# Optimization experiments

Measured on AMD Instinct MI355X. Metric: run time of the kernel, lower is better.

Reference implementation:

```python
import jax, jax.numpy as jnp
import numpy as np

H = 1024
NH = 16
HD = H // NH

def setup_inputs() -> dict:
    key = jax.random.key(0)
    ks = jax.random.split(key, 10)
    s = 1.0 / np.sqrt(H)
    return {
        "hiddenStates": jax.random.normal(ks[0], (2, 2048, H), dtype=jnp.float32),
        "attentionMask": jnp.zeros((2, 1, 1, 2048), dtype=jnp.float32),
        "Wq": jax.random.uniform(ks[1], (H, H), jnp.float32, -s, s),
        "bq": jax.random.uniform(ks[2], (H,), jnp.float32, -s, s),
        "Wk": jax.random.uniform(ks[3], (H, H), jnp.float32, -s, s),
        "bk": jax.random.uniform(ks[4], (H,), jnp.float32, -s, s),
        "Wv": jax.random.uniform(ks[5], (H, H), jnp.float32, -s, s),
        "bv": jax.random.uniform(ks[6], (H,), jnp.float32, -s, s),
        "Wo": jax.random.uniform(ks[7], (H, H), jnp.float32, -s, s),
        "bo": jax.random.uniform(ks[8], (H,), jnp.float32, -s, s),
    }

def _split_heads(x):
    # [B,S,H] -> [B,NH,S,HD]
    b, s, _ = x.shape
    return x.reshape(b, s, NH, HD).transpose(0, 2, 1, 3)

def reference(hiddenStates, attentionMask, Wq, bq, Wk, bk, Wv, bv, Wo, bo):
    q = _split_heads(hiddenStates @ Wq.T + bq)
    k = _split_heads(hiddenStates @ Wk.T + bk)
    v = _split_heads(hiddenStates @ Wv.T + bv)
    scores = jnp.einsum('bhqd,bhkd->bhqk', q, k) / np.sqrt(HD)
    scores = scores + attentionMask
    probs = jax.nn.softmax(scores, axis=-1)  # dropout p=0 -> identity
    ctx = jnp.einsum('bhqk,bhkd->bhqd', probs, v)
    b, _, s, _ = ctx.shape
    ctx = ctx.transpose(0, 2, 1, 3).reshape(b, s, H)
    return ctx @ Wo.T + bo
```

## Files before the change

### kernel.cpp

```cpp
#include <hip/hip_runtime.h>


#define BB   2
#define SS   2048
#define HH   1024
#define NHH  16
#define HDD  64

#define LOG2E 1.4426950408889634f
#define C1    (0.125f * LOG2E)

typedef _Float16 h8 __attribute__((ext_vector_type(8)));
typedef float f32x4 __attribute__((ext_vector_type(4)));
typedef float f32x16 __attribute__((ext_vector_type(16)));
typedef unsigned short us8 __attribute__((ext_vector_type(8)));

static __device__ __forceinline__ unsigned short f2h(float f) {
  return __builtin_bit_cast(unsigned short, (_Float16)f);
}
static __device__ __forceinline__ f32x4 mfma16(us8 a, us8 b, f32x4 c) {
  return __builtin_amdgcn_mfma_f32_16x16x32_f16(
      __builtin_bit_cast(h8, a), __builtin_bit_cast(h8, b), c, 0, 0, 0);
}
static __device__ __forceinline__ f32x16 mfma32(us8 a, us8 b, f32x16 c) {
  return __builtin_amdgcn_mfma_f32_32x32x16_f16(
      __builtin_bit_cast(h8, a), __builtin_bit_cast(h8, b), c, 0, 0, 0);
}
static __device__ __forceinline__ void gload16(const void* g, void* l) {
  __builtin_amdgcn_global_load_lds(
      (const __attribute__((address_space(1))) unsigned int*)g,
      (__attribute__((address_space(3))) unsigned int*)l, 16, 0, 0);
}
static __device__ __forceinline__ float exp2fast(float x) {
  float r; asm("v_exp_f32 %0, %1" : "=v"(r) : "v"(x)); return r;
}
static __device__ __forceinline__ unsigned cvtpkh(float lo, float hi) {
  unsigned r;
  asm("v_cvt_pkrtz_f16_f32 %0, %1, %2" : "=v"(r) : "v"(lo), "v"(hi));
  return r;
}
static __device__ __forceinline__ int fragoff(int lg, int r) {
  return (((lg << 10) + (r << 3)) ^ (lg << 3));
}

__global__ __launch_bounds__(256)
void pack_kernel(const float* __restrict__ X, const float* __restrict__ Wq,
                 const float* __restrict__ Wk, const float* __restrict__ Wv,
                 const float* __restrict__ Wo,
                 unsigned short* __restrict__ Xh,
                 unsigned short* __restrict__ Bh,
                 unsigned short* __restrict__ Oh) {
  const int t = blockIdx.x;
  const float* src; unsigned short* dst;
  int smt, dmt, kt;
  if (t < 1024) { src = X; dst = Xh; smt = t >> 5; dmt = smt; kt = t & 31; }
  else {
    const int u = t - 1024, which = u >> 8, v = u & 255;
    smt = v >> 5; kt = v & 31;
    if (which == 0)      { src = Wq; dst = Bh; dmt = smt; }
    else if (which == 1) { src = Wk; dst = Bh; dmt = smt + 8; }
    else if (which == 2) { src = Wv; dst = Bh; dmt = smt + 16; }
    else                 { src = Wo; dst = Oh; dmt = smt; }
  }
  const size_t tb = ((size_t)(dmt * 32 + kt)) << 12;
#pragma unroll
  for (int it = 0; it < 2; ++it) {
    const int item = it * 256 + threadIdx.x;
    const int r = item >> 2, lg = item & 3;
    const float* sp = &src[(size_t)(smt * 128 + r) * HH + kt * 32 + lg * 8];
    const float4 a = *(const float4*)sp;
    const float4 b = *(const float4*)(sp + 4);
    const float vals[8] = {a.x, a.y, a.z, a.w, b.x, b.y, b.z, b.w};
    us8 h;
#pragma unroll
    for (int e = 0; e < 8; ++e) h[e] = f2h(vals[e]);
    *(us8*)&dst[tb + fragoff(lg, r)] = h;
  }
}

__global__ __launch_bounds__(256, 3)
void qkv_gemm_kernel(const unsigned short* __restrict__ Ah_,
                     const unsigned short* __restrict__ Bh_,
                     const float* __restrict__ bq, const float* __restrict__ bk,
                     const float* __restrict__ bv,
                     unsigned short* __restrict__ qb,
                     unsigned short* __restrict__ kb,
                     unsigned short* __restrict__ vt) {
  __shared__ __align__(16) unsigned short tiles[2][4096];
  const int tid = threadIdx.x, lane = tid & 63, wid = tid >> 6;
  const int l16 = lane & 15, lg = lane >> 4;
  const int wr = wid >> 1, wc = wid & 1;
  const int mt0 = blockIdx.y, nt0 = blockIdx.x;

  const unsigned short* gA = Ah_ + (((size_t)mt0 * 32) << 12);
  const unsigned short* gB = Bh_ + (((size_t)nt0 * 32) << 12);

  f32x4 acc[4][4] = {};
  for (int kt = 0; kt < 32; ++kt) {
    __syncthreads();
    const size_t ko = ((size_t)kt) << 12;
#pragma unroll
    for (int it = 0; it < 2; ++it) {
      const int c = it * 256 + tid;
      gload16(gA + ko + c * 8, (char*)&tiles[0][0] + c * 16);
      gload16(gB + ko + c * 8, (char*)&tiles[1][0] + c * 16);
    }
    __syncthreads();

    us8 a[4], b[4];
#pragma unroll
    for (int t = 0; t < 4; ++t) {
      a[t] = *(const us8*)&tiles[0][fragoff(lg, wr * 64 + t * 16 + l16)];
      b[t] = *(const us8*)&tiles[1][fragoff(lg, wc * 64 + t * 16 + l16)];
    }
#pragma unroll
    for (int mt = 0; mt < 4; ++mt)
#pragma unroll
      for (int nt = 0; nt < 4; ++nt)
        acc[mt][nt] = mfma16(a[mt], b[nt], acc[mt][nt]);
  }

  const int m0 = mt0 * 128, n0 = nt0 * 128;
#pragma unroll
  for (int nt = 0; nt < 4; ++nt) {
    const int col = n0 + wc * 64 + nt * 16 + l16;
    const int which = col >> 10, nn = col & 1023;
    const float bias = (which == 0) ? bq[nn] : ((which == 1) ? bk[nn] : bv[nn]);
    const int h = nn >> 6, d = nn & 63;
#pragma unroll
    for (int mt = 0; mt < 4; ++mt)
#pragma unroll
      for (int reg = 0; reg < 4; ++reg) {
        const int row = m0 + wr * 64 + mt * 16 + lg * 4 + reg;
        const int bi = row >> 11, si = row & 2047;
        const unsigned short v16 = f2h(acc[mt][nt][reg] + bias);
        const size_t head = (size_t)(bi * NHH + h);
        if (which == 0)      qb[(head * SS + si) * HDD + d] = v16;
        else if (which == 1) kb[(head * SS + si) * HDD + d] = v16;
        else                 vt[(head * HDD + d) * SS + si] = v16;
      }
  }
}

__global__ __launch_bounds__(512)
void attn_kernel(const unsigned short* __restrict__ qb,
                 const unsigned short* __restrict__ kbuf,
                 const unsigned short* __restrict__ vt,
                 const float* __restrict__ mask,
                 unsigned short* __restrict__ Ch) {
  __shared__ __align__(16) unsigned short Klds[2][4096];
  __shared__ __align__(16) unsigned short Vlds[2][4096];

  const int tid = threadIdx.x, lane = tid & 63, w = tid >> 6;
  const int q = lane & 31, hi = lane >> 5;
  const int bh = blockIdx.x;
  const int bi = bh >> 4, h = bh & 15;
  const int q0 = blockIdx.y * 256 + w * 32;
  const size_t bhS = (size_t)bh * SS;
  const int qrow = q0 + q;

  us8 qf[4];
#pragma unroll
  for (int ks = 0; ks < 4; ++ks)
    qf[ks] = *(const us8*)&qb[(bhS + qrow) * HDD + ks * 16 + hi * 8];

  f32x16 o0 = {}, o1 = {};
  float mrun = -1e30f, lrun = 0.0f;

#define STAGE(buf, kt_)                                                        \
  {                                                                            \
    const int key0_ = (kt_) * 64;                                              \
    const int row_ = tid >> 3;                                                 \
    const int c16_ = (tid & 7) ^ (row_ & 7);          \
    gload16(&kbuf[(bhS + key0_ + row_) * HDD + c16_ * 8],                      \
            (char*)&Klds[buf][0] + tid * 16);                                  \
    gload16(&vt[((size_t)bh * HDD + row_) * SS + key0_ + c16_ * 8],            \
            (char*)&Vlds[buf][0] + tid * 16);                                  \
  }

  STAGE(0, 0)
  __syncthreads();

  for (int kt = 0; kt < SS / 64; ++kt) {
    const int buf = kt & 1;
    if (kt + 1 < SS / 64) STAGE(buf ^ 1, kt + 1)
    const int key0 = kt * 64;

    f32x16 s0 = {}, s1 = {};
    __builtin_amdgcn_s_setprio(1);
#pragma unroll
    for (int ks = 0; ks < 4; ++ks) {
      const int bc = ks * 32 + hi * 16;
      const char* kb0 = (const char*)&Klds[buf][0];
      const us8 kf0 = *(const us8*)(kb0 + q * 128 + (bc ^ ((q & 7) << 4)));
      const int r1 = 32 + q;
      const us8 kf1 = *(const us8*)(kb0 + r1 * 128 + (bc ^ ((r1 & 7) << 4)));
      s0 = mfma32(kf0, qf[ks], s0);
      s1 = mfma32(kf1, qf[ks], s1);
    }
    __builtin_amdgcn_s_setprio(0);

    float tmax = -1e30f;
#pragma unroll
    for (int g = 0; g < 4; ++g) {
      const float4 m0 = *(const float4*)&mask[bi * SS + key0 + g * 8 + hi * 4];
      const float4 m1 = *(const float4*)&mask[bi * SS + key0 + 32 + g * 8 + hi * 4];
      const float mm0[4] = {m0.x, m0.y, m0.z, m0.w};
      const float mm1[4] = {m1.x, m1.y, m1.z, m1.w};
#pragma unroll
      for (int j = 0; j < 4; ++j) {
        const int reg = g * 4 + j;
        s0[reg] = s0[reg] * C1 + mm0[j] * LOG2E;
        s1[reg] = s1[reg] * C1 + mm1[j] * LOG2E;
        tmax = fmaxf(tmax, fmaxf(s0[reg], s1[reg]));
      }
    }
    tmax = fmaxf(tmax, __shfl_xor(tmax, 32));

    const float mnew = fmaxf(mrun, tmax);
    if (!__all(tmax <= mrun)) {
      const float rsc = exp2fast(mrun - mnew);
      lrun *= rsc;
#pragma unroll
      for (int reg = 0; reg < 16; ++reg) { o0[reg] *= rsc; o1[reg] *= rsc; }
      mrun = mnew;
    }
    const float mb = mnew - 8.0f;
    float ps = 0.0f;
#pragma unroll
    for (int reg = 0; reg < 16; ++reg) {
      s0[reg] = exp2fast(s0[reg] - mb); ps += s0[reg];
      s1[reg] = exp2fast(s1[reg] - mb); ps += s1[reg];
    }
    ps += __shfl_xor(ps, 32);
    lrun += ps;

    us8 pb[4];
    {
      unsigned C[8], Sx[8];
#pragma unroll
      for (int j = 0; j < 8; ++j) C[j] = cvtpkh(s0[2 * j], s0[2 * j + 1]);
#pragma unroll
      for (int j = 0; j < 8; ++j) Sx[j] = (unsigned)__shfl_xor((int)C[j], 32);
      union { unsigned wd[4]; us8 v; } u0, u1;
      u0.wd[0] = hi ? Sx[2] : C[0]; u0.wd[1] = hi ? Sx[3] : C[1];
      u0.wd[2] = hi ? C[2] : Sx[0]; u0.wd[3] = hi ? C[3] : Sx[1];
      u1.wd[0] = hi ? Sx[6] : C[4]; u1.wd[1] = hi ? Sx[7] : C[5];
      u1.wd[2] = hi ? C[6] : Sx[4]; u1.wd[3] = hi ? C[7] : Sx[5];
      pb[0] = u0.v; pb[1] = u1.v;
#pragma unroll
      for (int j = 0; j < 8; ++j) C[j] = cvtpkh(s1[2 * j], s1[2 * j + 1]);
#pragma unroll
      for (int j = 0; j < 8; ++j) Sx[j] = (unsigned)__shfl_xor((int)C[j], 32);
      u0.wd[0] = hi ? Sx[2] : C[0]; u0.wd[1] = hi ? Sx[3] : C[1];
      u0.wd[2] = hi ? C[2] : Sx[0]; u0.wd[3] = hi ? C[3] : Sx[1];
      u1.wd[0] = hi ? Sx[6] : C[4]; u1.wd[1] = hi ? Sx[7] : C[5];
      u1.wd[2] = hi ? C[6] : Sx[4]; u1.wd[3] = hi ? C[7] : Sx[5];
      pb[2] = u0.v; pb[3] = u1.v;
    }

    __builtin_amdgcn_s_setprio(1);
#pragma unroll
    for (int kslice = 0; kslice < 4; ++kslice) {
      const int bc = kslice * 32 + hi * 16;
      const char* vb = (const char*)&Vlds[buf][0];
      const us8 vf0 = *(const us8*)(vb + q * 128 + (bc ^ ((q & 7) << 4)));
      const int r1 = 32 + q;
      const us8 vf1 = *(const us8*)(vb + r1 * 128 + (bc ^ ((r1 & 7) << 4)));
      o0 = mfma32(vf0, pb[kslice], o0);
      o1 = mfma32(vf1, pb[kslice], o1);
    }
    __builtin_amdgcn_s_setprio(0);

    __syncthreads();
  }

  const float rinv = 1.0f / lrun;
  const int m = bi * SS + qrow;
  const int mt = m >> 7, r = m & 127;
#pragma unroll
  for (int db = 0; db < 2; ++db) {
#pragma unroll
    for (int g = 0; g < 4; ++g) {
      const int d0 = db * 32 + g * 8 + hi * 4;
      const int col = h * 64 + d0;
      const int kt2 = col >> 5, lg2 = (col >> 3) & 3, e0 = col & 7;
      const size_t off = (((size_t)(mt * 32 + kt2)) << 12) + fragoff(lg2, r) + e0;
      ushort4 hv;
#pragma unroll
      for (int j = 0; j < 4; ++j)
        ((unsigned short*)&hv)[j] =
            f2h((db ? o1[g * 4 + j] : o0[g * 4 + j]) * rinv);
      *(ushort4*)&Ch[off] = hv;
    }
  }
#undef STAGE
}

__global__ __launch_bounds__(256, 3)
void out_gemm_kernel(const unsigned short* __restrict__ Ah_,
                     const unsigned short* __restrict__ Bh_,
                     const float* __restrict__ bo, float* __restrict__ out) {
  __shared__ __align__(16) unsigned short tiles[2][4096];
  const int tid = threadIdx.x, lane = tid & 63, wid = tid >> 6;
  const int l16 = lane & 15, lg = lane >> 4;
  const int wr = wid >> 1, wc = wid & 1;
  const int mt0 = blockIdx.y, nt0 = blockIdx.x;

  const unsigned short* gA = Ah_ + (((size_t)mt0 * 32) << 12);
  const unsigned short* gB = Bh_ + (((size_t)nt0 * 32) << 12);

  f32x4 acc[4][4] = {};
  for (int kt = 0; kt < 32; ++kt) {
    __syncthreads();
    const size_t ko = ((size_t)kt) << 12;
#pragma unroll
    for (int it = 0; it < 2; ++it) {
      const int c = it * 256 + tid;
      gload16(gA + ko + c * 8, (char*)&tiles[0][0] + c * 16);
      gload16(gB + ko + c * 8, (char*)&tiles[1][0] + c * 16);
    }
    __syncthreads();

    us8 a[4], b[4];
#pragma unroll
    for (int t = 0; t < 4; ++t) {
      a[t] = *(const us8*)&tiles[0][fragoff(lg, wr * 64 + t * 16 + l16)];
      b[t] = *(const us8*)&tiles[1][fragoff(lg, wc * 64 + t * 16 + l16)];
    }
#pragma unroll
    for (int mt = 0; mt < 4; ++mt)
#pragma unroll
      for (int nt = 0; nt < 4; ++nt)
        acc[mt][nt] = mfma16(a[mt], b[nt], acc[mt][nt]);
  }

  const int m0 = mt0 * 128, n0 = nt0 * 128;
#pragma unroll
  for (int nt = 0; nt < 4; ++nt) {
    const int col = n0 + wc * 64 + nt * 16 + l16;
    const float bias = bo[col];
#pragma unroll
    for (int mt = 0; mt < 4; ++mt)
#pragma unroll
      for (int reg = 0; reg < 4; ++reg) {
        const int row = m0 + wr * 64 + mt * 16 + lg * 4 + reg;
        out[(size_t)row * HH + col] = acc[mt][nt][reg] + bias;
      }
  }
}

extern "C" void kernel_launch(void* const* d_in, const int* in_sizes, int n_in,
                              void* d_out, int out_size, void* d_ws, size_t ws_size,
                              hipStream_t stream) {
  const float* X    = (const float*)d_in[0];
  const float* mask = (const float*)d_in[1];
  const float* Wq   = (const float*)d_in[2];
  const float* bq   = (const float*)d_in[3];
  const float* Wk   = (const float*)d_in[4];
  const float* bk   = (const float*)d_in[5];
  const float* Wv   = (const float*)d_in[6];
  const float* bv   = (const float*)d_in[7];
  const float* Wo   = (const float*)d_in[8];
  const float* bo   = (const float*)d_in[9];
  float* out = (float*)d_out;

  unsigned char* w = (unsigned char*)d_ws;
  const size_t MB = 1024 * 1024;
  unsigned short* Xh = (unsigned short*)(w);
  unsigned short* Bh = (unsigned short*)(w + 8 * MB);
  unsigned short* Oh = (unsigned short*)(w + 14 * MB);
  unsigned short* qb = (unsigned short*)(w + 16 * MB);
  unsigned short* kb = (unsigned short*)(w + 24 * MB);
  unsigned short* vt = (unsigned short*)(w + 32 * MB);
  unsigned short* Ch = Xh;

  pack_kernel<<<2048, 256, 0, stream>>>(X, Wq, Wk, Wv, Wo, Xh, Bh, Oh);
  qkv_gemm_kernel<<<dim3(24, 32), 256, 0, stream>>>(Xh, Bh, bq, bk, bv,
                                                    qb, kb, vt);
  attn_kernel<<<dim3(32, 8), 512, 0, stream>>>(qb, kb, vt, mask, Ch);
  out_gemm_kernel<<<dim3(8, 32), 256, 0, stream>>>(Ch, Oh, bo, out);
}
```

Before: 233.4 us.

## Split attention over key halves with combine kernel, stage mask in LDS

Splits the attention key range into two halves, doubling the attention grid from 256 to 512 blocks. Each half writes partial normalized outputs plus running max and sum, and a new combine kernel merges them into the packed layout used by the output GEMM. Several smaller changes ride along: the mask is pre-scaled by log2e in the pack kernel and staged through LDS, the row max uses a tree reduction, P packing uses permlane32_swap instead of shuffles, and V stores are vectorized in the QKV epilogue. The extra kernel launch and the partial-result round trip through memory are the costs traded for better occupancy on a GPU with many compute units.

```diff
diff --git a/kernel.cpp b/kernel.cpp
--- a/kernel.cpp
+++ b/kernel.cpp
@@ -14,9 +14,13 @@
 typedef float f32x4 __attribute__((ext_vector_type(4)));
 typedef float f32x16 __attribute__((ext_vector_type(16)));
 typedef unsigned short us8 __attribute__((ext_vector_type(8)));
+typedef unsigned u32x2 __attribute__((ext_vector_type(2)));
 
 static __device__ __forceinline__ unsigned short f2h(float f) {
   return __builtin_bit_cast(unsigned short, (_Float16)f);
+}
+static __device__ __forceinline__ float h2f(unsigned short h) {
+  return (float)__builtin_bit_cast(_Float16, h);
 }
 static __device__ __forceinline__ f32x4 mfma16(us8 a, us8 b, f32x4 c) {
   return __builtin_amdgcn_mfma_f32_16x16x32_f16(
@@ -39,6 +43,10 @@
   asm("v_cvt_pkrtz_f16_f32 %0, %1, %2" : "=v"(r) : "v"(lo), "v"(hi));
   return r;
 }
+static __device__ __forceinline__ void pl32swap(unsigned& a, unsigned& b) {
+  u32x2 r = __builtin_amdgcn_permlane32_swap(a, b, false, false);
+  a = r[0]; b = r[1];
+}
 static __device__ __forceinline__ int fragoff(int lg, int r) {
   return (((lg << 10) + (r << 3)) ^ (lg << 3));
 }
@@ -46,11 +54,22 @@
 __global__ __launch_bounds__(256)
 void pack_kernel(const float* __restrict__ X, const float* __restrict__ Wq,
                  const float* __restrict__ Wk, const float* __restrict__ Wv,
-                 const float* __restrict__ Wo,
+                 const float* __restrict__ Wo, const float* __restrict__ mask,
                  unsigned short* __restrict__ Xh,
                  unsigned short* __restrict__ Bh,
-                 unsigned short* __restrict__ Oh) {
+                 unsigned short* __restrict__ Oh,
+                 float* __restrict__ maskl) {
   const int t = blockIdx.x;
+  if (t == 2048) {
+    const int i0 = threadIdx.x * 16;
+#pragma unroll
+    for (int j = 0; j < 4; ++j) {
+      float4 v = *(const float4*)&mask[i0 + j * 4];
+      v.x *= LOG2E; v.y *= LOG2E; v.z *= LOG2E; v.w *= LOG2E;
+      *(float4*)&maskl[i0 + j * 4] = v;
+    }
+    return;
+  }
   const float* src; unsigned short* dst;
   int smt, dmt, kt;
   if (t < 1024) { src = X; dst = Xh; smt = t >> 5; dmt = smt; kt = t & 31; }
@@ -128,17 +147,25 @@
     const float bias = (which == 0) ? bq[nn] : ((which == 1) ? bk[nn] : bv[nn]);
     const int h = nn >> 6, d = nn & 63;
 #pragma unroll
-    for (int mt = 0; mt < 4; ++mt)
-#pragma unroll
-      for (int reg = 0; reg < 4; ++reg) {
-        const int row = m0 + wr * 64 + mt * 16 + lg * 4 + reg;
-        const int bi = row >> 11, si = row & 2047;
-        const unsigned short v16 = f2h(acc[mt][nt][reg] + bias);
-        const size_t head = (size_t)(bi * NHH + h);
-        if (which == 0)      qb[(head * SS + si) * HDD + d] = v16;
-        else if (which == 1) kb[(head * SS + si) * HDD + d] = v16;
-        else                 vt[(head * HDD + d) * SS + si] = v16;
+    for (int mt = 0; mt < 4; ++mt) {
+      const int row0 = m0 + wr * 64 + mt * 16 + lg * 4;
+      const int bi = row0 >> 11, si0 = row0 & 2047;
+      const size_t head = (size_t)(bi * NHH + h);
+      if (which == 2) {
+        ushort4 vv;
+#pragma unroll
+        for (int reg = 0; reg < 4; ++reg)
+          ((unsigned short*)&vv)[reg] = f2h(acc[mt][nt][reg] + bias);
+        *(ushort4*)&vt[(head * HDD + d) * SS + si0] = vv;
+      } else {
+#pragma unroll
+        for (int reg = 0; reg < 4; ++reg) {
+          const unsigned short v16 = f2h(acc[mt][nt][reg] + bias);
+          if (which == 0) qb[(head * SS + si0 + reg) * HDD + d] = v16;
+          else            kb[(head * SS + si0 + reg) * HDD + d] = v16;
+        }
       }
+    }
   }
 }
 
@@ -146,16 +173,20 @@
 void attn_kernel(const unsigned short* __restrict__ qb,
                  const unsigned short* __restrict__ kbuf,
                  const unsigned short* __restrict__ vt,
-                 const float* __restrict__ mask,
-                 unsigned short* __restrict__ Ch) {
+                 const float* __restrict__ maskl,
+                 unsigned short* __restrict__ Op,
+                 float2* __restrict__ Ml) {
   __shared__ __align__(16) unsigned short Klds[2][4096];
   __shared__ __align__(16) unsigned short Vlds[2][4096];
+  __shared__ __align__(16) float Mlds[2][64];
 
   const int tid = threadIdx.x, lane = tid & 63, w = tid >> 6;
   const int q = lane & 31, hi = lane >> 5;
   const int bh = blockIdx.x;
   const int bi = bh >> 4, h = bh & 15;
-  const int q0 = blockIdx.y * 256 + w * 32;
+  const int half = blockIdx.y >> 3;
+  const int q0 = (blockIdx.y & 7) * 256 + w * 32;
+  const int kbase = half * (SS / 2);
   const size_t bhS = (size_t)bh * SS;
   const int qrow = q0 + q;
 
@@ -169,22 +200,24 @@
 
 #define STAGE(buf, kt_)                                                        \
   {                                                                            \
-    const int key0_ = (kt_) * 64;                                              \
+    const int key0_ = kbase + (kt_) * 64;                                      \
     const int row_ = tid >> 3;                                                 \
     const int c16_ = (tid & 7) ^ (row_ & 7);          \
     gload16(&kbuf[(bhS + key0_ + row_) * HDD + c16_ * 8],                      \
             (char*)&Klds[buf][0] + tid * 16);                                  \
     gload16(&vt[((size_t)bh * HDD + row_) * SS + key0_ + c16_ * 8],            \
             (char*)&Vlds[buf][0] + tid * 16);                                  \
+    if (tid < 16)                                                              \
+      gload16(&maskl[bi * SS + key0_ + tid * 4],                               \
+              (char*)&Mlds[buf][0] + tid * 16);                                \
   }
 
   STAGE(0, 0)
   __syncthreads();
 
-  for (int kt = 0; kt < SS / 64; ++kt) {
+  for (int kt = 0; kt < 16; ++kt) {
     const int buf = kt & 1;
-    if (kt + 1 < SS / 64) STAGE(buf ^ 1, kt + 1)
-    const int key0 = kt * 64;
+    if (kt + 1 < 16) STAGE(buf ^ 1, kt + 1)
 
     f32x16 s0 = {}, s1 = {};
     __builtin_amdgcn_s_setprio(1);
@@ -200,21 +233,25 @@
     }
     __builtin_amdgcn_s_setprio(0);
 
-    float tmax = -1e30f;
+    float mx0[8], mx1[4];
 #pragma unroll
     for (int g = 0; g < 4; ++g) {
-      const float4 m0 = *(const float4*)&mask[bi * SS + key0 + g * 8 + hi * 4];
-      const float4 m1 = *(const float4*)&mask[bi * SS + key0 + 32 + g * 8 + hi * 4];
-      const float mm0[4] = {m0.x, m0.y, m0.z, m0.w};
-      const float mm1[4] = {m1.x, m1.y, m1.z, m1.w};
+      const float4 m0v = *(const float4*)&Mlds[buf][g * 8 + hi * 4];
+      const float4 m1v = *(const float4*)&Mlds[buf][32 + g * 8 + hi * 4];
+      const float mm0[4] = {m0v.x, m0v.y, m0v.z, m0v.w};
+      const float mm1[4] = {m1v.x, m1v.y, m1v.z, m1v.w};
 #pragma unroll
       for (int j = 0; j < 4; ++j) {
         const int reg = g * 4 + j;
-        s0[reg] = s0[reg] * C1 + mm0[j] * LOG2E;
-        s1[reg] = s1[reg] * C1 + mm1[j] * LOG2E;
-        tmax = fmaxf(tmax, fmaxf(s0[reg], s1[reg]));
+        s0[reg] = s0[reg] * C1 + mm0[j];
+        s1[reg] = s1[reg] * C1 + mm1[j];
       }
-    }
+      mx0[2 * g]     = fmaxf(fmaxf(s0[g * 4], s0[g * 4 + 1]), s0[g * 4 + 2]);
+      mx0[2 * g + 1] = fmaxf(fmaxf(s1[g * 4], s1[g * 4 + 1]), s1[g * 4 + 2]);
+      mx1[g] = fmaxf(fmaxf(s0[g * 4 + 3], s1[g * 4 + 3]),
+                     fmaxf(mx0[2 * g], mx0[2 * g + 1]));
+    }
+    float tmax = fmaxf(fmaxf(mx1[0], mx1[1]), fmaxf(mx1[2], mx1[3]));
     tmax = fmaxf(tmax, __shfl_xor(tmax, 32));
 
     const float mnew = fmaxf(mrun, tmax);
@@ -237,25 +274,21 @@
 
     us8 pb[4];
     {
-      unsigned C[8], Sx[8];
+      unsigned C[8];
 #pragma unroll
       for (int j = 0; j < 8; ++j) C[j] = cvtpkh(s0[2 * j], s0[2 * j + 1]);
-#pragma unroll
-      for (int j = 0; j < 8; ++j) Sx[j] = (unsigned)__shfl_xor((int)C[j], 32);
+      pl32swap(C[0], C[2]); pl32swap(C[1], C[3]);
+      pl32swap(C[4], C[6]); pl32swap(C[5], C[7]);
       union { unsigned wd[4]; us8 v; } u0, u1;
-      u0.wd[0] = hi ? Sx[2] : C[0]; u0.wd[1] = hi ? Sx[3] : C[1];
-      u0.wd[2] = hi ? C[2] : Sx[0]; u0.wd[3] = hi ? C[3] : Sx[1];
-      u1.wd[0] = hi ? Sx[6] : C[4]; u1.wd[1] = hi ? Sx[7] : C[5];
-      u1.wd[2] = hi ? C[6] : Sx[4]; u1.wd[3] = hi ? C[7] : Sx[5];
+      u0.wd[0] = C[0]; u0.wd[1] = C[1]; u0.wd[2] = C[2]; u0.wd[3] = C[3];
+      u1.wd[0] = C[4]; u1.wd[1] = C[5]; u1.wd[2] = C[6]; u1.wd[3] = C[7];
       pb[0] = u0.v; pb[1] = u1.v;
 #pragma unroll
       for (int j = 0; j < 8; ++j) C[j] = cvtpkh(s1[2 * j], s1[2 * j + 1]);
-#pragma unroll
-      for (int j = 0; j < 8; ++j) Sx[j] = (unsigned)__shfl_xor((int)C[j], 32);
-      u0.wd[0] = hi ? Sx[2] : C[0]; u0.wd[1] = hi ? Sx[3] : C[1];
-      u0.wd[2] = hi ? C[2] : Sx[0]; u0.wd[3] = hi ? C[3] : Sx[1];
-      u1.wd[0] = hi ? Sx[6] : C[4]; u1.wd[1] = hi ? Sx[7] : C[5];
-      u1.wd[2] = hi ? C[6] : Sx[4]; u1.wd[3] = hi ? C[7] : Sx[5];
+      pl32swap(C[0], C[2]); pl32swap(C[1], C[3]);
+      pl32swap(C[4], C[6]); pl32swap(C[5], C[7]);
+      u0.wd[0] = C[0]; u0.wd[1] = C[1]; u0.wd[2] = C[2]; u0.wd[3] = C[3];
+      u1.wd[0] = C[4]; u1.wd[1] = C[5]; u1.wd[2] = C[6]; u1.wd[3] = C[7];
       pb[2] = u0.v; pb[3] = u1.v;
     }
 
@@ -275,26 +308,64 @@
     __syncthreads();
   }
 
-  const float rinv = 1.0f / lrun;
-  const int m = bi * SS + qrow;
-  const int mt = m >> 7, r = m & 127;
-#pragma unroll
-  for (int db = 0; db < 2; ++db) {
-#pragma unroll
-    for (int g = 0; g < 4; ++g) {
-      const int d0 = db * 32 + g * 8 + hi * 4;
-      const int col = h * 64 + d0;
-      const int kt2 = col >> 5, lg2 = (col >> 3) & 3, e0 = col & 7;
-      const size_t off = (((size_t)(mt * 32 + kt2)) << 12) + fragoff(lg2, r) + e0;
-      ushort4 hv;
-#pragma unroll
-      for (int j = 0; j < 4; ++j)
-        ((unsigned short*)&hv)[j] =
-            f2h((db ? o1[g * 4 + j] : o0[g * 4 + j]) * rinv);
-      *(ushort4*)&Ch[off] = hv;
-    }
-  }
+  const float linv = (lrun > 0.0f) ? 1.0f / lrun : 0.0f;
+  unsigned short* op = Op + (((size_t)half * 32 + bh) * SS + qrow) * HDD;
+#pragma unroll
+  for (int g = 0; g < 4; ++g) {
+    ushort4 v0, v1;
+#pragma unroll
+    for (int j = 0; j < 4; ++j) {
+      ((unsigned short*)&v0)[j] = f2h(o0[g * 4 + j] * linv);
+      ((unsigned short*)&v1)[j] = f2h(o1[g * 4 + j] * linv);
+    }
+    *(ushort4*)&op[g * 8 + hi * 4]      = v0;
+    *(ushort4*)&op[32 + g * 8 + hi * 4] = v1;
+  }
+  if (hi == 0)
+    Ml[((size_t)half * 32 + bh) * SS + qrow] = float2{mrun, lrun};
 #undef STAGE
+}
+
+__global__ __launch_bounds__(256)
+void combine_kernel(const unsigned short* __restrict__ Op,
+                    const float2* __restrict__ Ml,
+                    unsigned short* __restrict__ Ch) {
+  const int gid = blockIdx.x * 256 + threadIdx.x;
+  const int row = gid >> 2, qtr = gid & 3;
+  const int bh = row >> 11, s = row & 2047;
+  const int bi = bh >> 4, h = bh & 15;
+
+  const float2 ml0 = Ml[row];
+  const float2 ml1 = Ml[(size_t)65536 + row];
+  const float m = fmaxf(ml0.x, ml1.x);
+  float w0 = ml0.y * exp2fast(ml0.x - m);
+  float w1 = ml1.y * exp2fast(ml1.x - m);
+  const float tot = w0 + w1;
+  const float rinv = (tot > 0.0f) ? 1.0f / tot : 0.0f;
+  w0 *= rinv; w1 *= rinv;
+
+  const int d0 = qtr * 16;
+  const us8* p0 = (const us8*)&Op[(size_t)row * HDD + d0];
+  const us8* p1 = (const us8*)&Op[(size_t)65536 * HDD + (size_t)row * HDD + d0];
+  const us8 a0 = p0[0], a1 = p0[1], b0 = p1[0], b1 = p1[1];
+
+  const int mrow = bi * SS + s;
+  const int mt = mrow >> 7, r = mrow & 127;
+#pragma unroll
+  for (int j4 = 0; j4 < 4; ++j4) {
+    const int col = h * 64 + d0 + j4 * 4;
+    const int kt2 = col >> 5, lg2 = (col >> 3) & 3, e0 = col & 7;
+    const size_t off = (((size_t)(mt * 32 + kt2)) << 12) + fragoff(lg2, r) + e0;
+    ushort4 hv;
+#pragma unroll
+    for (int j = 0; j < 4; ++j) {
+      const int k = j4 * 4 + j;
+      const float va = h2f(k < 8 ? a0[k] : a1[k - 8]);
+      const float vb = h2f(k < 8 ? b0[k] : b1[k - 8]);
+      ((unsigned short*)&hv)[j] = f2h(va * w0 + vb * w1);
+    }
+    *(ushort4*)&Ch[off] = hv;
+  }
 }
 
 __global__ __launch_bounds__(256, 3)
@@ -373,11 +444,16 @@
   unsigned short* qb = (unsigned short*)(w + 16 * MB);
   unsigned short* kb = (unsigned short*)(w + 24 * MB);
   unsigned short* vt = (unsigned short*)(w + 32 * MB);
+  unsigned short* Op = (unsigned short*)(w + 40 * MB);
+  float2*         Ml = (float2*)(w + 56 * MB);
+  float*       maskl = (float*)(w + 57 * MB);
   unsigned short* Ch = Xh;
 
-  pack_kernel<<<2048, 256, 0, stream>>>(X, Wq, Wk, Wv, Wo, Xh, Bh, Oh);
+  pack_kernel<<<2049, 256, 0, stream>>>(X, Wq, Wk, Wv, Wo, mask,
+                                        Xh, Bh, Oh, maskl);
   qkv_gemm_kernel<<<dim3(24, 32), 256, 0, stream>>>(Xh, Bh, bq, bk, bv,
                                                     qb, kb, vt);
-  attn_kernel<<<dim3(32, 8), 512, 0, stream>>>(qb, kb, vt, mask, Ch);
+  attn_kernel<<<dim3(32, 16), 512, 0, stream>>>(qb, kb, vt, maskl, Op, Ml);
+  combine_kernel<<<1024, 256, 0, stream>>>(Op, Ml, Ch);
   out_gemm_kernel<<<dim3(8, 32), 256, 0, stream>>>(Ch, Oh, bo, out);
 }
```

After: 202.0 us. 13.4% less time.
